# Optimization experiments

Hardware: AMD Instinct MI355X
Metric: run time of the kernel (lower is better)

The kernel has to match this reference:

```python
import jax, jax.numpy as jnp
import numpy as np

D_MODEL = 512
N_HEADS = 8
D_HEAD = D_MODEL // N_HEADS
N_BINS = 32


def setup_inputs() -> dict:
    key = jax.random.key(0)
    ks = jax.random.split(key, 12)
    B, N = 8, 1024
    x = jax.random.normal(ks[0], (B, N, D_MODEL), dtype=jnp.float32)
    positions = jax.random.randint(ks[1], (B, N), 0, 5000, dtype=jnp.int32)
    mask = jnp.ones((B, N), dtype=jnp.float32)
    s = 0.02
    qw = jax.random.normal(ks[2], (D_MODEL, D_MODEL), jnp.float32) * s
    qb = jnp.zeros((D_MODEL,), jnp.float32)
    kw = jax.random.normal(ks[3], (D_MODEL, D_MODEL), jnp.float32) * s
    kb = jnp.zeros((D_MODEL,), jnp.float32)
    vw = jax.random.normal(ks[4], (D_MODEL, D_MODEL), jnp.float32) * s
    vb = jnp.zeros((D_MODEL,), jnp.float32)
    ow = jax.random.normal(ks[5], (D_MODEL, D_MODEL), jnp.float32) * s
    ob = jnp.zeros((D_MODEL,), jnp.float32)
    dist_emb = jax.random.normal(ks[6], (N_BINS, N_HEADS), jnp.float32) * s
    order_bias = jnp.zeros((N_HEADS,), jnp.float32)
    bin_edges = jnp.logspace(0.0, 3.0, N_BINS - 1, dtype=jnp.float32)
    return {"x": x, "positions": positions, "mask": mask,
            "qw": qw, "qb": qb, "kw": kw, "kb": kb, "vw": vw, "vb": vb,
            "ow": ow, "ob": ob, "dist_emb": dist_emb, "order_bias": order_bias,
            "bin_edges": bin_edges}


def reference(x, positions, mask, qw, qb, kw, kb, vw, vb, ow, ob, dist_emb, order_bias, bin_edges):
    B, N, _ = x.shape
    scale = jnp.sqrt(jnp.float32(D_HEAD))
    # projections (torch Linear: y = x @ W^T + b), split heads -> (B,H,N,Dh)
    q = (x @ qw.T + qb).reshape(B, N, N_HEADS, D_HEAD).transpose(0, 2, 1, 3)
    k = (x @ kw.T + kb).reshape(B, N, N_HEADS, D_HEAD).transpose(0, 2, 1, 3)
    v = (x @ vw.T + vb).reshape(B, N, N_HEADS, D_HEAD).transpose(0, 2, 1, 3)
    scores = jnp.einsum('bhqd,bhkd->bhqk', q, k) / scale  # (B,H,N,N)
    pos = positions.astype(jnp.float32)
    pos_i = pos[:, :, None]   # (B,N,1)
    pos_j = pos[:, None, :]   # (B,1,N)
    dist = jnp.abs(pos_j - pos_i)  # (B,N,N)
    # torch.bucketize(right=False) == searchsorted side='left'
    bins = jnp.clip(jnp.searchsorted(bin_edges, dist, side='left'), 0, N_BINS - 1)
    dist_bias = dist_emb[bins]  # (B,N,N,H)
    scores = scores + dist_bias.transpose(0, 3, 1, 2)
    order_sign = (pos_j > pos_i).astype(scores.dtype) - 0.5  # (B,N,N)
    scores = scores + order_sign[:, None, :, :] * order_bias[None, :, None, None]
    mask_2d = mask[:, None, None, :] * mask[:, None, :, None]  # (B,1,N,N)
    scores = jnp.where(mask_2d == 0, jnp.float32(-1e9), scores)
    attn = jax.nn.softmax(scores, axis=-1)
    attn = jnp.nan_to_num(attn, nan=0.0)
    out = jnp.einsum('bhqk,bhkd->bhqd', attn, v)
    out = out.transpose(0, 2, 1, 3).reshape(B, N, D_MODEL)
    out = out * mask[..., None]
    return out @ ow.T + ob
```

## Files before the change

kernel.cpp:

```cpp
#include <hip/hip_runtime.h>
#include <hip/hip_bf16.h>

#define SEQ   1024
#define NH    8
#define DH    64

typedef __attribute__((ext_vector_type(8))) _Float16 half8;
typedef __attribute__((ext_vector_type(4))) _Float16 half4;
typedef __attribute__((ext_vector_type(4))) float    f32x4;

#if __has_builtin(__builtin_amdgcn_exp2f)
#define EXP2F __builtin_amdgcn_exp2f
#else
#define EXP2F exp2f
#endif

__device__ inline unsigned pk2(float a, float b) {
  return __builtin_bit_cast(unsigned, __builtin_amdgcn_cvt_pkrtz(a, b));
}
__device__ inline void swap32(unsigned &a, unsigned &b) {
  asm("v_permlane32_swap_b32 %0, %1" : "+v"(a), "+v"(b));
}
__device__ inline void swap16(unsigned &a, unsigned &b) {
  asm("v_permlane16_swap_b32 %0, %1" : "+v"(a), "+v"(b));
}
__device__ inline half8 mk8(unsigned a, unsigned b, unsigned c, unsigned d) {
  union { unsigned u[4]; half8 h; } x;
  x.u[0] = a; x.u[1] = b; x.u[2] = c; x.u[3] = d;
  return x.h;
}
__device__ __forceinline__ void gload16(const _Float16* g, _Float16* l) {
  __builtin_amdgcn_global_load_lds((const __attribute__((address_space(1))) void*)g,
                                   (__attribute__((address_space(3))) void*)l, 16, 0, 0);
}

#define BARRIER4 do {                                        \
    __builtin_amdgcn_sched_barrier(0);                       \
    asm volatile("s_waitcnt vmcnt(4)" ::: "memory");         \
    __builtin_amdgcn_s_barrier();                            \
    __builtin_amdgcn_sched_barrier(0);                       \
  } while (0)

__global__ void prep_all(const float* __restrict__ x,
                         const float* __restrict__ qw, const float* __restrict__ kw,
                         const float* __restrict__ vw, const float* __restrict__ ow,
                         const float* __restrict__ qb, const float* __restrict__ kb,
                         const float* __restrict__ vb, const float* __restrict__ edges,
                         _Float16* __restrict__ xh, _Float16* __restrict__ wqkvh,
                         _Float16* __restrict__ owh, float* __restrict__ qkvbias,
                         unsigned char* __restrict__ lutd) {
  const int blk = blockIdx.x, tid = threadIdx.x;
  if (blk < 4096) {
    int g = blk * 256 + tid;
    float4 v = reinterpret_cast<const float4*>(x)[g];
    half4 u;
    u[0] = (_Float16)v.x; u[1] = (_Float16)v.y; u[2] = (_Float16)v.z; u[3] = (_Float16)v.w;
    reinterpret_cast<half4*>(xh)[g] = u;
  } else if (blk < 5122) {
    int g = (blk - 4096) * 256 + tid;
    if (g < 196608) {
      const float* src = (g < 65536) ? qw : (g < 131072) ? kw : vw;
      int lg = g & 65535;
      float4 v = reinterpret_cast<const float4*>(src)[lg];
      half4 u;
      u[0] = (_Float16)v.x; u[1] = (_Float16)v.y; u[2] = (_Float16)v.z; u[3] = (_Float16)v.w;
      reinterpret_cast<half4*>(wqkvh)[g] = u;
    } else if (g < 262144) {
      int lg = g - 196608;
      float4 v = reinterpret_cast<const float4*>(ow)[lg];
      half4 u;
      u[0] = (_Float16)v.x; u[1] = (_Float16)v.y; u[2] = (_Float16)v.z; u[3] = (_Float16)v.w;
      reinterpret_cast<half4*>(owh)[lg] = u;
    } else if (g < 262528) {
      int lg = g - 262144;
      const float* src = (lg < 128) ? qb : (lg < 256) ? kb : vb;
      int ll = lg & 127;
      reinterpret_cast<float4*>(qkvbias)[lg] = reinterpret_cast<const float4*>(src)[ll];
    }
  } else {
    int d = (blk - 5122) * 256 + tid;
    float fd = (float)d;
    int bin = 0;
#pragma unroll
    for (int t = 0; t < 31; ++t) bin += (edges[t] < fd) ? 1 : 0;
    lutd[d] = (unsigned char)bin;
  }
}

__global__ __launch_bounds__(256) void prep_ebins(const int* __restrict__ positions,
                                                  const float* __restrict__ mask,
                                                  const unsigned char* __restrict__ lutd,
                                                  unsigned char* __restrict__ ebins) {
  __shared__ unsigned char lutl[5120];
  __shared__ int posl[SEQ];
  __shared__ unsigned char mk[SEQ];
  const int b = blockIdx.x >> 8, j0 = (blockIdx.x & 255) * 4;
  const int tid = threadIdx.x;
  for (int i = tid; i < 1280; i += 256)
    reinterpret_cast<unsigned*>(lutl)[i] = reinterpret_cast<const unsigned*>(lutd)[i];
  for (int i = tid; i < SEQ; i += 256) {
    posl[i] = positions[b * SEQ + i];
    mk[i] = (mask[b * SEQ + i] == 0.f) ? 32 : 0;
  }
  __syncthreads();
  const int c0 = tid * 4;
#pragma unroll
  for (int jj = 0; jj < 4; ++jj) {
    const int j = j0 + jj;
    const int pr = posl[j];
    unsigned out = 0;
#pragma unroll
    for (int r = 0; r < 4; ++r) {
      int c = c0 + r;
      int pc = posl[c];
      int d = pc - pr; d = d < 0 ? -d : d;
      if (d > 5119) d = 5119;
      unsigned e = lutl[d] | (unsigned)mk[c] | ((pc > pr) ? 64u : 0u);
      out |= e << (8 * r);
    }
    reinterpret_cast<unsigned*>(&ebins[(size_t)(b * SEQ + j) * SEQ])[tid] = out;
  }
}

__global__ __launch_bounds__(256) void qkv_gemm3(const _Float16* __restrict__ xh,
                                                 const _Float16* __restrict__ wh,
                                                 const float* __restrict__ bias,
                                                 _Float16* __restrict__ qkv) {
  __shared__ __attribute__((aligned(16))) _Float16 As[128 * 64];
  __shared__ __attribute__((aligned(16))) _Float16 Bs[128 * 64];
  const int m0 = blockIdx.x * 128, n0 = blockIdx.y * 128;
  const int tid = threadIdx.x, w = tid >> 6, lane = tid & 63;
  const int lr = lane & 15, lg = lane >> 4;
  const int wr = (w >> 1) * 64, wc = (w & 1) * 64;
  f32x4 acc[4][4] = {};
  const int srow8 = lane >> 3;
  const int scol = ((lane & 7) ^ srow8) * 8;
  for (int k0 = 0; k0 < 512; k0 += 64) {
#pragma unroll
    for (int j = 0; j < 4; ++j) {
      const int row = (w * 4 + j) * 8 + srow8;
      gload16(&xh[(size_t)(m0 + row) * 512 + k0 + scol], &As[(w * 4 + j) * 512]);
      gload16(&wh[(size_t)(n0 + row) * 512 + k0 + scol], &Bs[(w * 4 + j) * 512]);
    }
    __syncthreads();
#pragma unroll
    for (int kk = 0; kk < 2; ++kk) {
      half8 af[4], bf[4];
#pragma unroll
      for (int mt = 0; mt < 4; ++mt) {
        const int row = wr + mt * 16 + lr;
        af[mt] = *reinterpret_cast<const half8*>(
            (const char*)As + row * 128 + (((kk * 4 + lg) ^ (row & 7)) * 16));
      }
#pragma unroll
      for (int nt = 0; nt < 4; ++nt) {
        const int row = wc + nt * 16 + lr;
        bf[nt] = *reinterpret_cast<const half8*>(
            (const char*)Bs + row * 128 + (((kk * 4 + lg) ^ (row & 7)) * 16));
      }
#pragma unroll
      for (int mt = 0; mt < 4; ++mt)
#pragma unroll
        for (int nt = 0; nt < 4; ++nt)
          acc[mt][nt] = __builtin_amdgcn_mfma_f32_16x16x32_f16(af[mt], bf[nt], acc[mt][nt], 0, 0, 0);
    }
    __syncthreads();
  }
  const int p = n0 >> 9;
  const float scl = (p == 0) ? 0.125f : (p == 1) ? 1.44269504f : 1.0f;
  if (p < 2) {
#pragma unroll
    for (int nt = 0; nt < 4; ++nt) {
      int n = n0 + wc + nt * 16 + lr;
      float bv = bias[n];
      int c = n & 511, h = c >> 6, d = c & 63;
#pragma unroll
      for (int mt = 0; mt < 4; ++mt)
#pragma unroll
        for (int r = 0; r < 4; ++r) {
          int m = m0 + wr + mt * 16 + lg * 4 + r;
          int bb = m >> 10, nn = m & 1023;
          qkv[p * 4194304 + ((bb * NH + h) * SEQ + nn) * DH + d] = (_Float16)((acc[mt][nt][r] + bv) * scl);
        }
    }
  } else {
#pragma unroll
    for (int nt = 0; nt < 4; ++nt) {
      int n = n0 + wc + nt * 16 + lr;
      float bv = bias[n];
      int c = n & 511, h = c >> 6, d = c & 63;
#pragma unroll
      for (int mt = 0; mt < 4; ++mt) {
        int m = m0 + wr + mt * 16 + lg * 4;
        int bb = m >> 10, nn = m & 1023;
        half4 st;
#pragma unroll
        for (int r = 0; r < 4; ++r) st[r] = (_Float16)(acc[mt][nt][r] + bv);
        *reinterpret_cast<half4*>(&qkv[8388608 + ((bb * NH + h) * DH + d) * SEQ + nn]) = st;
      }
    }
  }
}

#define ASTAGE(bufi, kv0_) do {                                                              \
    _Pragma("unroll") for (int j = 0; j < 2; ++j) {                                          \
      const int row_ = (w * 2 + j) * 8 + (lane >> 3);                                        \
      const int c_ = ((lane & 7) ^ (row_ & 7)) * 8;                                          \
      gload16(Kg + (size_t)((kv0_) + row_) * 64 + c_, &Ks[bufi][(w * 2 + j) * 512]);         \
      gload16(Vtg + (size_t)row_ * 1024 + (kv0_) + c_, &Vt[bufi][(w * 2 + j) * 512]);        \
    }                                                                                        \
  } while (0)

#define EBL(dst, kt_) do {                                                                   \
    _Pragma("unroll") for (int ct = 0; ct < 4; ++ct)                                         \
      dst[ct] = *reinterpret_cast<const unsigned*>(                                          \
          &ebins[(size_t)(b * SEQ + q_base + lr) * SEQ + (kt_) * 64 + ct * 16 + lg * 4]);    \
  } while (0)

#define ACOMP(bufi, ebw) do {                                                                \
    f32x4 s[4];                                                                              \
    _Pragma("unroll") for (int ct = 0; ct < 4; ++ct) {                                       \
      const unsigned eb_ = ebw[ct];                                                          \
      _Pragma("unroll") for (int r = 0; r < 4; ++r) {                                        \
        const unsigned i6_ = (eb_ >> (8 * r)) & 63u;                      \
        float bias_ = elut2[i6_];                                                            \
        if (obh_nz) bias_ += ((eb_ >> (8 * r)) & 64u) ? obh : -obh;                          \
        s[ct][r] = bias_;                                                                    \
      }                                                                                      \
    }                                                                                        \
    __builtin_amdgcn_s_setprio(1);                                                           \
    _Pragma("unroll") for (int ct = 0; ct < 4; ++ct) {                                       \
      const int krow_ = ct * 16 + lr;                                                        \
      half8 kf0 = *reinterpret_cast<const half8*>(                                           \
          (const char*)&Ks[bufi][0] + krow_ * 128 + ((lg ^ (krow_ & 7)) * 16));              \
      half8 kf1 = *reinterpret_cast<const half8*>(                                           \
          (const char*)&Ks[bufi][0] + krow_ * 128 + (((4 + lg) ^ (krow_ & 7)) * 16));        \
      s[ct] = __builtin_amdgcn_mfma_f32_16x16x32_f16(kf0, qf[0], s[ct], 0, 0, 0);            \
      s[ct] = __builtin_amdgcn_mfma_f32_16x16x32_f16(kf1, qf[1], s[ct], 0, 0, 0);            \
    }                                                                                        \
    __builtin_amdgcn_s_setprio(0);                                                           \
                 \
    unsigned W[4][2];                                                                        \
    _Pragma("unroll") for (int ct = 0; ct < 4; ++ct) {                                       \
      float p0 = EXP2F(s[ct][0]), p1 = EXP2F(s[ct][1]);                                      \
      float p2 = EXP2F(s[ct][2]), p3 = EXP2F(s[ct][3]);                                      \
      l_run += (p0 + p1) + (p2 + p3);                                                        \
      W[ct][0] = pk2(p0, p1);                                                                \
      W[ct][1] = pk2(p2, p3);                                                                \
    }                                                                                        \
    swap32(W[0][0], W[1][0]); swap32(W[0][1], W[1][1]);                                      \
    swap32(W[2][0], W[3][0]); swap32(W[2][1], W[3][1]);                                      \
    swap16(W[0][0], W[1][0]); swap16(W[0][1], W[1][1]);                                      \
    swap16(W[2][0], W[3][0]); swap16(W[2][1], W[3][1]);                                      \
    __builtin_amdgcn_s_setprio(1);                                                           \
    _Pragma("unroll") for (int ks = 0; ks < 2; ++ks) {                                       \
      half8 pa = mk8(W[ks * 2][0], W[ks * 2][1], W[ks * 2 + 1][0], W[ks * 2 + 1][1]);        \
      _Pragma("unroll") for (int dt = 0; dt < 4; ++dt) {                                     \
        const int vrow_ = dt * 16 + lr;                                                      \
        half8 vf = *reinterpret_cast<const half8*>(                                          \
            (const char*)&Vt[bufi][0] + vrow_ * 128 + (((ks * 4 + lg) ^ (vrow_ & 7)) * 16)); \
        o[dt] = __builtin_amdgcn_mfma_f32_16x16x32_f16(vf, pa, o[dt], 0, 0, 0);              \
      }                                                                                      \
    }                                                                                        \
    __builtin_amdgcn_s_setprio(0);                                                           \
  } while (0)

__global__ __launch_bounds__(256, 4) void attn9(const _Float16* __restrict__ qkv,
                                                const float* __restrict__ mask,
                                                const unsigned char* __restrict__ ebins,
                                                const float* __restrict__ demb,
                                                const float* __restrict__ obias,
                                                _Float16* __restrict__ aout) {
  __shared__ __attribute__((aligned(16))) _Float16 Ks[2][64 * 64];
  __shared__ __attribute__((aligned(16))) _Float16 Vt[2][64 * 64];
  __shared__ float elut2[64];

  const int blk = blockIdx.x;
  const int lin = (blk & 7) * 128 + (blk >> 3);
  const int qt = lin & 15, h = (lin >> 4) & 7, b = lin >> 7;
  const int tid = threadIdx.x, w = tid >> 6, lane = tid & 63;
  const int lr = lane & 15, lg = lane >> 4;

  if (tid < 64) elut2[tid] = (tid < 32) ? demb[tid * NH + h] * 1.44269504f : -1.442695e9f;
  const float obh = 0.5f * obias[h] * 1.44269504f;
  const bool obh_nz = (obh != 0.f);

  const _Float16* Qg  = qkv + (size_t)(b * NH + h) * 65536;
  const _Float16* Kg  = qkv + 4194304 + (size_t)(b * NH + h) * 65536;
  const _Float16* Vtg = qkv + 8388608 + (size_t)(b * NH + h) * 65536;

  const int q_base = qt * 64 + w * 16;
  half8 qf[2];
#pragma unroll
  for (int ks = 0; ks < 2; ++ks)
    qf[ks] = *reinterpret_cast<const half8*>(&Qg[(q_base + lr) * DH + ks * 32 + lg * 8]);
  const float mq = mask[b * SEQ + q_base + lr];

  float l_run = 0.f;
  f32x4 o[4] = {};

  unsigned ebwA[4], ebwB[4];
  ASTAGE(0, 0);
  EBL(ebwA, 0);
  __syncthreads();

#pragma unroll 1
  for (int i = 0; i < 8; ++i) {
    const int kt = 2 * i;
    ASTAGE(1, (kt + 1) * 64);
    EBL(ebwB, kt + 1);
    ACOMP(0, ebwA);
    BARRIER4;
    if (kt + 2 < 16) {
      ASTAGE(0, (kt + 2) * 64);
      EBL(ebwA, kt + 2);
    }
    ACOMP(1, ebwB);
    BARRIER4;
  }

  float s_ = l_run;
  s_ += __shfl_xor(s_, 16);
  s_ += __shfl_xor(s_, 32);
  const float linv = mq / fmaxf(s_, 1e-35f);
#pragma unroll
  for (int dt = 0; dt < 4; ++dt) {
    half4 st;
#pragma unroll
    for (int r = 0; r < 4; ++r) st[r] = (_Float16)(o[dt][r] * linv);
    *reinterpret_cast<half4*>(
        &aout[(size_t)(b * SEQ + q_base + lr) * 512 + h * DH + dt * 16 + lg * 4]) = st;
  }
}

__global__ __launch_bounds__(256) void out_gemm3(const _Float16* __restrict__ ah,
                                                 const _Float16* __restrict__ wh,
                                                 const float* __restrict__ ob,
                                                 float* __restrict__ out) {
  __shared__ __attribute__((aligned(16))) _Float16 As[128 * 64];
  __shared__ __attribute__((aligned(16))) _Float16 Bs[64 * 64];
  const int m0 = blockIdx.x * 128, n0 = blockIdx.y * 64;
  const int tid = threadIdx.x, w = tid >> 6, lane = tid & 63;
  const int lr = lane & 15, lg = lane >> 4;
  const int wr = (w >> 1) * 64, wc = (w & 1) * 32;
  f32x4 acc[4][2] = {};
  const int srow8 = lane >> 3;
  const int scol = ((lane & 7) ^ srow8) * 8;
  for (int k0 = 0; k0 < 512; k0 += 64) {
#pragma unroll
    for (int j = 0; j < 4; ++j) {
      const int row = (w * 4 + j) * 8 + srow8;
      gload16(&ah[(size_t)(m0 + row) * 512 + k0 + scol], &As[(w * 4 + j) * 512]);
    }
#pragma unroll
    for (int j = 0; j < 2; ++j) {
      const int row = (w * 2 + j) * 8 + srow8;
      gload16(&wh[(size_t)(n0 + row) * 512 + k0 + scol], &Bs[(w * 2 + j) * 512]);
    }
    __syncthreads();
#pragma unroll
    for (int kk = 0; kk < 2; ++kk) {
      half8 af[4], bf[2];
#pragma unroll
      for (int mt = 0; mt < 4; ++mt) {
        const int row = wr + mt * 16 + lr;
        af[mt] = *reinterpret_cast<const half8*>(
            (const char*)As + row * 128 + (((kk * 4 + lg) ^ (row & 7)) * 16));
      }
#pragma unroll
      for (int nt = 0; nt < 2; ++nt) {
        const int row = wc + nt * 16 + lr;
        bf[nt] = *reinterpret_cast<const half8*>(
            (const char*)Bs + row * 128 + (((kk * 4 + lg) ^ (row & 7)) * 16));
      }
#pragma unroll
      for (int mt = 0; mt < 4; ++mt)
#pragma unroll
        for (int nt = 0; nt < 2; ++nt)
          acc[mt][nt] = __builtin_amdgcn_mfma_f32_16x16x32_f16(af[mt], bf[nt], acc[mt][nt], 0, 0, 0);
    }
    __syncthreads();
  }
#pragma unroll
  for (int nt = 0; nt < 2; ++nt) {
    int n = n0 + wc + nt * 16 + lr;
    float bv = ob[n];
#pragma unroll
    for (int mt = 0; mt < 4; ++mt)
#pragma unroll
      for (int r = 0; r < 4; ++r) {
        int m = m0 + wr + mt * 16 + lg * 4 + r;
        out[m * 512 + n] = acc[mt][nt][r] + bv;
      }
  }
}

extern "C" void kernel_launch(void* const* d_in, const int* in_sizes, int n_in,
                              void* d_out, int out_size, void* d_ws, size_t ws_size,
                              hipStream_t stream) {
  const float* x         = (const float*)d_in[0];
  const int*   positions = (const int*)d_in[1];
  const float* mask      = (const float*)d_in[2];
  const float* qw        = (const float*)d_in[3];
  const float* qb        = (const float*)d_in[4];
  const float* kw        = (const float*)d_in[5];
  const float* kb        = (const float*)d_in[6];
  const float* vw        = (const float*)d_in[7];
  const float* vb        = (const float*)d_in[8];
  const float* ow        = (const float*)d_in[9];
  const float* ob        = (const float*)d_in[10];
  const float* demb      = (const float*)d_in[11];
  const float* obias     = (const float*)d_in[12];
  const float* edges     = (const float*)d_in[13];

  char* ws = (char*)d_ws;
  _Float16* xh        = (_Float16*)(ws);
  unsigned char* ebins = (unsigned char*)(ws);
  _Float16* qkv       = (_Float16*)(ws + 8388608);
  _Float16* aouth     = (_Float16*)(ws + 33554432);
  _Float16* wqkvh     = (_Float16*)(ws + 41943040);
  _Float16* owh       = (_Float16*)(ws + 43515904);
  float*    qkvbias   = (float*)(ws + 44040192);
  unsigned char* lutd = (unsigned char*)(ws + 44046336);
  float*    outp      = (float*)d_out;

  prep_all<<<5142, 256, 0, stream>>>(x, qw, kw, vw, ow, qb, kb, vb, edges,
                                     xh, wqkvh, owh, qkvbias, lutd);
  qkv_gemm3<<<dim3(64, 12), 256, 0, stream>>>(xh, wqkvh, qkvbias, qkv);
  prep_ebins<<<2048, 256, 0, stream>>>(positions, mask, lutd, ebins);
  attn9<<<1024, 256, 0, stream>>>(qkv, mask, ebins, demb, obias, aouth);
  out_gemm3<<<dim3(64, 8), 256, 0, stream>>>(aouth, owh, ob, outp);
}
```

Baseline: 102.0 us.

## Double-buffer GEMM K-tiles, remap block order, and read K directly from global

Both projection GEMMs now use two 32-wide K stages in shared memory, so the next tile loads while the current one is multiplied, with a single barrier per half-step. Block indices are remapped into a linearized order that groups blocks, which should improve L2 reuse. In attention, K fragments are read straight from global memory instead of being staged through LDS, freeing shared memory and removing one async copy per tile. The cost is uncoalesced 16-byte K reads from global/L2 inside the MFMA loop, and more barriers in the GEMMs.

```diff
diff --git a/kernel.cpp b/kernel.cpp
--- a/kernel.cpp
+++ b/kernel.cpp
@@ -122,50 +122,60 @@
   }
 }
 
-__global__ __launch_bounds__(256) void qkv_gemm3(const _Float16* __restrict__ xh,
+#define QGSTAGE(bi, k0_) do {                                                                \
+    _Pragma("unroll") for (int j2 = 0; j2 < 2; ++j2) {                                       \
+      const int j_ = w * 2 + j2;                                                             \
+      const int row_ = j_ * 16 + (lane >> 2);                                                \
+      gload16(&xh[(size_t)(m0 + row_) * 512 + (k0_) + csrc], &As[bi][j_ * 512]);             \
+      gload16(&wh[(size_t)(n0 + row_) * 512 + (k0_) + csrc], &Bs[bi][j_ * 512]);             \
+    }                                                                                        \
+  } while (0)
+
+#define QCOMP(bi) do {                                                                       \
+    half8 af[4], bf[4];                                                                      \
+    _Pragma("unroll") for (int mt = 0; mt < 4; ++mt) {                                       \
+      const int row_ = wr + mt * 16 + lr;                                                    \
+      af[mt] = *reinterpret_cast<const half8*>(                                              \
+          (const char*)&As[bi][0] + row_ * 64 + ((lg ^ ((row_ >> 1) & 3)) * 16));            \
+    }                                                                                        \
+    _Pragma("unroll") for (int nt = 0; nt < 4; ++nt) {                                       \
+      const int row_ = wc + nt * 16 + lr;                                                    \
+      bf[nt] = *reinterpret_cast<const half8*>(                                              \
+          (const char*)&Bs[bi][0] + row_ * 64 + ((lg ^ ((row_ >> 1) & 3)) * 16));            \
+    }                                                                                        \
+    _Pragma("unroll") for (int mt = 0; mt < 4; ++mt)                                         \
+      _Pragma("unroll") for (int nt = 0; nt < 4; ++nt)                                       \
+        acc[mt][nt] = __builtin_amdgcn_mfma_f32_16x16x32_f16(af[mt], bf[nt], acc[mt][nt], 0, 0, 0); \
+  } while (0)
+
+__global__ __launch_bounds__(256) void qkv_gemm5(const _Float16* __restrict__ xh,
                                                  const _Float16* __restrict__ wh,
                                                  const float* __restrict__ bias,
                                                  _Float16* __restrict__ qkv) {
-  __shared__ __attribute__((aligned(16))) _Float16 As[128 * 64];
-  __shared__ __attribute__((aligned(16))) _Float16 Bs[128 * 64];
-  const int m0 = blockIdx.x * 128, n0 = blockIdx.y * 128;
+  __shared__ __attribute__((aligned(16))) _Float16 As[2][128 * 32];
+  __shared__ __attribute__((aligned(16))) _Float16 Bs[2][128 * 32];
+  const int blk = blockIdx.x;
+  const int lin = (blk & 7) * 96 + (blk >> 3);
+  const int bx = lin / 12, by = lin % 12;
+  const int m0 = bx * 128, n0 = by * 128;
   const int tid = threadIdx.x, w = tid >> 6, lane = tid & 63;
   const int lr = lane & 15, lg = lane >> 4;
   const int wr = (w >> 1) * 64, wc = (w & 1) * 64;
   f32x4 acc[4][4] = {};
-  const int srow8 = lane >> 3;
-  const int scol = ((lane & 7) ^ srow8) * 8;
-  for (int k0 = 0; k0 < 512; k0 += 64) {
-#pragma unroll
-    for (int j = 0; j < 4; ++j) {
-      const int row = (w * 4 + j) * 8 + srow8;
-      gload16(&xh[(size_t)(m0 + row) * 512 + k0 + scol], &As[(w * 4 + j) * 512]);
-      gload16(&wh[(size_t)(n0 + row) * 512 + k0 + scol], &Bs[(w * 4 + j) * 512]);
-    }
+  const int csrc = (((lane & 3) ^ ((lane >> 3) & 3))) * 8;
+
+  QGSTAGE(0, 0);
+  __syncthreads();
+#pragma unroll 1
+  for (int i = 0; i < 8; ++i) {
+    QGSTAGE(1, i * 64 + 32);
+    QCOMP(0);
     __syncthreads();
-#pragma unroll
-    for (int kk = 0; kk < 2; ++kk) {
-      half8 af[4], bf[4];
-#pragma unroll
-      for (int mt = 0; mt < 4; ++mt) {
-        const int row = wr + mt * 16 + lr;
-        af[mt] = *reinterpret_cast<const half8*>(
-            (const char*)As + row * 128 + (((kk * 4 + lg) ^ (row & 7)) * 16));
-      }
-#pragma unroll
-      for (int nt = 0; nt < 4; ++nt) {
-        const int row = wc + nt * 16 + lr;
-        bf[nt] = *reinterpret_cast<const half8*>(
-            (const char*)Bs + row * 128 + (((kk * 4 + lg) ^ (row & 7)) * 16));
-      }
-#pragma unroll
-      for (int mt = 0; mt < 4; ++mt)
-#pragma unroll
-        for (int nt = 0; nt < 4; ++nt)
-          acc[mt][nt] = __builtin_amdgcn_mfma_f32_16x16x32_f16(af[mt], bf[nt], acc[mt][nt], 0, 0, 0);
-    }
+    if (i < 7) QGSTAGE(0, i * 64 + 64);
+    QCOMP(1);
     __syncthreads();
   }
+
   const int p = n0 >> 9;
   const float scl = (p == 0) ? 0.125f : (p == 1) ? 1.44269504f : 1.0f;
   if (p < 2) {
@@ -206,7 +216,6 @@
     _Pragma("unroll") for (int j = 0; j < 2; ++j) {                                          \
       const int row_ = (w * 2 + j) * 8 + (lane >> 3);                                        \
       const int c_ = ((lane & 7) ^ (row_ & 7)) * 8;                                          \
-      gload16(Kg + (size_t)((kv0_) + row_) * 64 + c_, &Ks[bufi][(w * 2 + j) * 512]);         \
       gload16(Vtg + (size_t)row_ * 1024 + (kv0_) + c_, &Vt[bufi][(w * 2 + j) * 512]);        \
     }                                                                                        \
   } while (0)
@@ -217,7 +226,7 @@
           &ebins[(size_t)(b * SEQ + q_base + lr) * SEQ + (kt_) * 64 + ct * 16 + lg * 4]);    \
   } while (0)
 
-#define ACOMP(bufi, ebw) do {                                                                \
+#define ACOMP(bufi, ebw, kv0_) do {                                                          \
     f32x4 s[4];                                                                              \
     _Pragma("unroll") for (int ct = 0; ct < 4; ++ct) {                                       \
       const unsigned eb_ = ebw[ct];                                                          \
@@ -230,11 +239,9 @@
     }                                                                                        \
     __builtin_amdgcn_s_setprio(1);                                                           \
     _Pragma("unroll") for (int ct = 0; ct < 4; ++ct) {                                       \
-      const int krow_ = ct * 16 + lr;                                                        \
-      half8 kf0 = *reinterpret_cast<const half8*>(                                           \
-          (const char*)&Ks[bufi][0] + krow_ * 128 + ((lg ^ (krow_ & 7)) * 16));              \
-      half8 kf1 = *reinterpret_cast<const half8*>(                                           \
-          (const char*)&Ks[bufi][0] + krow_ * 128 + (((4 + lg) ^ (krow_ & 7)) * 16));        \
+      const size_t kro_ = (size_t)((kv0_) + ct * 16 + lr) * 64;                              \
+      half8 kf0 = *reinterpret_cast<const half8*>(&Kg[kro_ + lg * 8]);                       \
+      half8 kf1 = *reinterpret_cast<const half8*>(&Kg[kro_ + 32 + lg * 8]);                  \
       s[ct] = __builtin_amdgcn_mfma_f32_16x16x32_f16(kf0, qf[0], s[ct], 0, 0, 0);            \
       s[ct] = __builtin_amdgcn_mfma_f32_16x16x32_f16(kf1, qf[1], s[ct], 0, 0, 0);            \
     }                                                                                        \
@@ -265,13 +272,12 @@
     __builtin_amdgcn_s_setprio(0);                                                           \
   } while (0)
 
-__global__ __launch_bounds__(256, 4) void attn9(const _Float16* __restrict__ qkv,
-                                                const float* __restrict__ mask,
-                                                const unsigned char* __restrict__ ebins,
-                                                const float* __restrict__ demb,
-                                                const float* __restrict__ obias,
-                                                _Float16* __restrict__ aout) {
-  __shared__ __attribute__((aligned(16))) _Float16 Ks[2][64 * 64];
+__global__ __launch_bounds__(256, 4) void attn10(const _Float16* __restrict__ qkv,
+                                                 const float* __restrict__ mask,
+                                                 const unsigned char* __restrict__ ebins,
+                                                 const float* __restrict__ demb,
+                                                 const float* __restrict__ obias,
+                                                 _Float16* __restrict__ aout) {
   __shared__ __attribute__((aligned(16))) _Float16 Vt[2][64 * 64];
   __shared__ float elut2[64];
 
@@ -309,13 +315,13 @@
     const int kt = 2 * i;
     ASTAGE(1, (kt + 1) * 64);
     EBL(ebwB, kt + 1);
-    ACOMP(0, ebwA);
+    ACOMP(0, ebwA, kt * 64);
     BARRIER4;
     if (kt + 2 < 16) {
       ASTAGE(0, (kt + 2) * 64);
       EBL(ebwA, kt + 2);
     }
-    ACOMP(1, ebwB);
+    ACOMP(1, ebwB, (kt + 1) * 64);
     BARRIER4;
   }
 
@@ -333,52 +339,60 @@
   }
 }
 
-__global__ __launch_bounds__(256) void out_gemm3(const _Float16* __restrict__ ah,
+#define OGSTAGE(bi, k0_) do {                                                                \
+    _Pragma("unroll") for (int j2 = 0; j2 < 2; ++j2) {                                       \
+      const int j_ = w * 2 + j2;                                                             \
+      const int row_ = j_ * 16 + (lane >> 2);                                                \
+      gload16(&ah[(size_t)(m0 + row_) * 512 + (k0_) + csrc], &As[bi][j_ * 512]);             \
+    }                                                                                        \
+    {                                                                                        \
+      const int row_ = w * 16 + (lane >> 2);                                                 \
+      gload16(&wh[(size_t)(n0 + row_) * 512 + (k0_) + csrc], &Bs[bi][w * 512]);              \
+    }                                                                                        \
+  } while (0)
+
+#define OCOMP(bi) do {                                                                       \
+    half8 af[4], bf[2];                                                                      \
+    _Pragma("unroll") for (int mt = 0; mt < 4; ++mt) {                                       \
+      const int row_ = wr + mt * 16 + lr;                                                    \
+      af[mt] = *reinterpret_cast<const half8*>(                                              \
+          (const char*)&As[bi][0] + row_ * 64 + ((lg ^ ((row_ >> 1) & 3)) * 16));            \
+    }                                                                                        \
+    _Pragma("unroll") for (int nt = 0; nt < 2; ++nt) {                                       \
+      const int row_ = wc + nt * 16 + lr;                                                    \
+      bf[nt] = *reinterpret_cast<const half8*>(                                              \
+          (const char*)&Bs[bi][0] + row_ * 64 + ((lg ^ ((row_ >> 1) & 3)) * 16));            \
+    }                                                                                        \
+    _Pragma("unroll") for (int mt = 0; mt < 4; ++mt)                                         \
+      _Pragma("unroll") for (int nt = 0; nt < 2; ++nt)                                       \
+        acc[mt][nt] = __builtin_amdgcn_mfma_f32_16x16x32_f16(af[mt], bf[nt], acc[mt][nt], 0, 0, 0); \
+  } while (0)
+
+__global__ __launch_bounds__(256) void out_gemm5(const _Float16* __restrict__ ah,
                                                  const _Float16* __restrict__ wh,
                                                  const float* __restrict__ ob,
                                                  float* __restrict__ out) {
-  __shared__ __attribute__((aligned(16))) _Float16 As[128 * 64];
-  __shared__ __attribute__((aligned(16))) _Float16 Bs[64 * 64];
-  const int m0 = blockIdx.x * 128, n0 = blockIdx.y * 64;
+  __shared__ __attribute__((aligned(16))) _Float16 As[2][128 * 32];
+  __shared__ __attribute__((aligned(16))) _Float16 Bs[2][64 * 32];
+  const int blk = blockIdx.x;
+  const int lin = (blk & 7) * 64 + (blk >> 3);
+  const int bx = lin >> 3, by = lin & 7;
+  const int m0 = bx * 128, n0 = by * 64;
   const int tid = threadIdx.x, w = tid >> 6, lane = tid & 63;
   const int lr = lane & 15, lg = lane >> 4;
   const int wr = (w >> 1) * 64, wc = (w & 1) * 32;
   f32x4 acc[4][2] = {};
-  const int srow8 = lane >> 3;
-  const int scol = ((lane & 7) ^ srow8) * 8;
-  for (int k0 = 0; k0 < 512; k0 += 64) {
-#pragma unroll
-    for (int j = 0; j < 4; ++j) {
-      const int row = (w * 4 + j) * 8 + srow8;
-      gload16(&ah[(size_t)(m0 + row) * 512 + k0 + scol], &As[(w * 4 + j) * 512]);
-    }
-#pragma unroll
-    for (int j = 0; j < 2; ++j) {
-      const int row = (w * 2 + j) * 8 + srow8;
-      gload16(&wh[(size_t)(n0 + row) * 512 + k0 + scol], &Bs[(w * 2 + j) * 512]);
-    }
+  const int csrc = (((lane & 3) ^ ((lane >> 3) & 3))) * 8;
+
+  OGSTAGE(0, 0);
+  __syncthreads();
+#pragma unroll 1
+  for (int i = 0; i < 8; ++i) {
+    OGSTAGE(1, i * 64 + 32);
+    OCOMP(0);
     __syncthreads();
-#pragma unroll
-    for (int kk = 0; kk < 2; ++kk) {
-      half8 af[4], bf[2];
-#pragma unroll
-      for (int mt = 0; mt < 4; ++mt) {
-        const int row = wr + mt * 16 + lr;
-        af[mt] = *reinterpret_cast<const half8*>(
-            (const char*)As + row * 128 + (((kk * 4 + lg) ^ (row & 7)) * 16));
-      }
-#pragma unroll
-      for (int nt = 0; nt < 2; ++nt) {
-        const int row = wc + nt * 16 + lr;
-        bf[nt] = *reinterpret_cast<const half8*>(
-            (const char*)Bs + row * 128 + (((kk * 4 + lg) ^ (row & 7)) * 16));
-      }
-#pragma unroll
-      for (int mt = 0; mt < 4; ++mt)
-#pragma unroll
-        for (int nt = 0; nt < 2; ++nt)
-          acc[mt][nt] = __builtin_amdgcn_mfma_f32_16x16x32_f16(af[mt], bf[nt], acc[mt][nt], 0, 0, 0);
-    }
+    if (i < 7) OGSTAGE(0, i * 64 + 64);
+    OCOMP(1);
     __syncthreads();
   }
 #pragma unroll
@@ -426,8 +440,8 @@
 
   prep_all<<<5142, 256, 0, stream>>>(x, qw, kw, vw, ow, qb, kb, vb, edges,
                                      xh, wqkvh, owh, qkvbias, lutd);
-  qkv_gemm3<<<dim3(64, 12), 256, 0, stream>>>(xh, wqkvh, qkvbias, qkv);
+  qkv_gemm5<<<768, 256, 0, stream>>>(xh, wqkvh, qkvbias, qkv);
   prep_ebins<<<2048, 256, 0, stream>>>(positions, mask, lutd, ebins);
-  attn9<<<1024, 256, 0, stream>>>(qkv, mask, ebins, demb, obias, aouth);
-  out_gemm3<<<dim3(64, 8), 256, 0, stream>>>(aouth, owh, ob, outp);
-}
+  attn10<<<1024, 256, 0, stream>>>(qkv, mask, ebins, demb, obias, aouth);
+  out_gemm5<<<512, 256, 0, stream>>>(aouth, owh, ob, outp);
+}
```

After: 155.0 us. 1.52x slower.
